# Kernel optimization log

Hardware: AMD Instinct MI355X
Metric: run time of the kernel (lower is better)

The kernel has to match this reference:

```python
import jax, jax.numpy as jnp
import numpy as np

D_MODEL = 1024
N_HEADS = 16
HEAD_DIM = D_MODEL // N_HEADS
B, S = 2, 2048


def setup_inputs() -> dict:
    key = jax.random.key(0)
    k1, k2, k3, k4, k5 = jax.random.split(key, 5)
    scale = 1.0 / np.sqrt(D_MODEL)
    return {
        "x": jax.random.normal(k1, (B, S, D_MODEL), dtype=jnp.float32),
        "mask": jnp.ones((B, S), dtype=jnp.int32),
        "W_qkv": jax.random.normal(k2, (D_MODEL, 3 * D_MODEL), dtype=jnp.float32) * scale,
        "b_qkv": jnp.zeros((3 * D_MODEL,), dtype=jnp.float32),
        "W_proj": jax.random.normal(k3, (D_MODEL, D_MODEL), dtype=jnp.float32) * scale,
        "b_proj": jnp.zeros((D_MODEL,), dtype=jnp.float32),
    }


def reference(x, mask, W_qkv, b_qkv, W_proj, b_proj):
    b, s, d = x.shape
    qkv = x @ W_qkv + b_qkv                                  # [B,S,3D]
    qkv = qkv.reshape(b, s, 3, N_HEADS, HEAD_DIM)
    qkv = jnp.transpose(qkv, (2, 0, 3, 1, 4))                # [3,B,H,S,Dh]
    q, k, v = qkv[0], qkv[1], qkv[2]
    scores = jnp.einsum("bhqd,bhkd->bhqk", q, k) / np.sqrt(HEAD_DIM)
    if mask is not None:
        m = mask[:, None, None, :]                           # [B,1,1,S]
        scores = jnp.where(m == 0, -jnp.inf, scores)
    attn = jax.nn.softmax(scores, axis=-1)
    out = jnp.einsum("bhqk,bhkd->bhqd", attn, v)             # [B,H,S,Dh]
    out = jnp.transpose(out, (0, 2, 1, 3)).reshape(b, s, d)  # [B,S,D]
    return out @ W_proj + b_proj
```

## Files before the change

### kernel.cpp

```cpp
#include <hip/hip_runtime.h>

typedef unsigned short u16;
typedef unsigned int u32;
typedef __bf16 bf16x8 __attribute__((ext_vector_type(8)));
typedef float f32x4 __attribute__((ext_vector_type(4)));
typedef float f32x16 __attribute__((ext_vector_type(16)));

#define D_MODEL 1024
#define SQ 2048
#define NH 16
#define HD 64
#define QSCALE 0.1803368801111204f

__device__ __forceinline__ u16 f2bf(float f) {
    u32 u = __builtin_bit_cast(u32, f);
    u = (u + 0x7fffu + ((u >> 16) & 1u)) >> 16;
    return (u16)u;
}

__device__ __forceinline__ f32x4 mfma16(bf16x8 a, bf16x8 b, f32x4 c) {
    return __builtin_amdgcn_mfma_f32_16x16x32_bf16(a, b, c, 0, 0, 0);
}
__device__ __forceinline__ f32x16 mfma32(bf16x8 a, bf16x8 b, f32x16 c) {
    return __builtin_amdgcn_mfma_f32_32x32x16_bf16(a, b, c, 0, 0, 0);
}

__device__ __forceinline__ bf16x8 ld16(const void* p) {
    return __builtin_bit_cast(bf16x8, *(const int4*)p);
}

__device__ __forceinline__ void gl_lds16(const u16* g, u16* l) {
    __builtin_amdgcn_global_load_lds((const __attribute__((address_space(1))) unsigned int*)g,
                                     (__attribute__((address_space(3))) unsigned int*)l, 16, 0, 0);
}

__device__ __forceinline__ u32 cvtpk(float a, float b) {
    u32 r;
    asm("v_cvt_pk_bf16_f32 %0, %1, %2" : "=v"(r) : "v"(a), "v"(b));
    return r;
}

__device__ __forceinline__ void swap32(u32& a, u32& b) {
    asm("v_permlane32_swap_b32 %0, %1" : "+v"(a), "+v"(b));
}

__device__ __forceinline__ void barrier_fence() {
    asm volatile("s_barrier" ::: "memory");
}


__global__ __launch_bounds__(256) void prep(const float* __restrict__ x, u16* __restrict__ x_bf,
                                            const float* __restrict__ Wqkv, u16* __restrict__ wq_t,
                                            const float* __restrict__ Wproj, u16* __restrict__ wp_t) {
    __shared__ float t[32][33];
    const int bid = blockIdx.x, tid = threadIdx.x;

    if (bid < 1024) {
#pragma unroll
        for (int j = 0; j < 4; ++j) {
            int i = bid * 1024 + j * 256 + tid;
            float4 v = ((const float4*)x)[i];
            ushort4 o;
            o.x = f2bf(v.x); o.y = f2bf(v.y); o.z = f2bf(v.z); o.w = f2bf(v.w);
            ((ushort4*)x_bf)[i] = o;
        }
        return;
    }

    const float* in;
    u16* out;
    int K = 1024, N, tile;
    if (bid < 4096) {
        in = Wqkv; out = wq_t; N = 3072; tile = bid - 1024;
    } else {
        in = Wproj; out = wp_t; N = 1024; tile = bid - 4096;
    }
    const int nbx = N / 32;
    const int n0 = (tile % nbx) * 32, k0 = (tile / nbx) * 32;
    const int tx = tid & 31, ty = tid >> 5;
#pragma unroll
    for (int i = 0; i < 4; ++i)
        t[ty + 8 * i][tx] = in[(size_t)(k0 + ty + 8 * i) * N + n0 + tx];
    __syncthreads();
#pragma unroll
    for (int i = 0; i < 4; ++i)
        out[(size_t)(n0 + ty + 8 * i) * K + k0 + tx] = f2bf(t[tx][ty + 8 * i]);
}

__global__ __launch_bounds__(256) void vtrans(const u16* __restrict__ Vw, u16* __restrict__ Vtw) {
    __shared__ u16 T[64][72];
    const int bh = blockIdx.y, s0 = blockIdx.x * 64, tid = threadIdx.x;
    const int r = tid >> 3, cb = tid & 7;
#pragma unroll
    for (int i = 0; i < 2; ++i) {
        int rr = r + 32 * i;
        int4 v = *(const int4*)(Vw + ((size_t)bh * SQ + s0 + rr) * HD + cb * 8);
        *(int4*)&T[rr][cb * 8] = v;
    }
    __syncthreads();
#pragma unroll
    for (int i = 0; i < 2; ++i) {
        int d = r + 32 * i, so = cb * 8;
        u16 tmp[8];
#pragma unroll
        for (int j = 0; j < 8; ++j) tmp[j] = T[so + j][d];
        *(int4*)(Vtw + ((size_t)bh * HD + d) * SQ + s0 + so) = *(int4*)tmp;
    }
}


template <int MODE>
__global__ __launch_bounds__(256) void gemm128(const u16* __restrict__ A,
                                               const u16* __restrict__ Bt,
                                               const float* __restrict__ bias,
                                               u16* __restrict__ Qw, u16* __restrict__ Kw,
                                               u16* __restrict__ Vw, float* __restrict__ Out) {
    __shared__ u16 As[128 * 32];
    __shared__ u16 Bs[128 * 32];

    const int tid = threadIdx.x;
    const int l = tid & 63, w = tid >> 6;
    const int l16 = l & 15, lq = l >> 4;
    const int wm = w >> 1, wn = w & 1;
    const int m0 = blockIdx.y * 128, n0 = blockIdx.x * 128;

    f32x4 acc[4][4];
#pragma unroll
    for (int i = 0; i < 4; ++i)
#pragma unroll
        for (int j = 0; j < 4; ++j) acc[i][j] = f32x4{0.f, 0.f, 0.f, 0.f};

    const int srow = 32 * w + (l >> 2);
    const u16* aSrc = A + (size_t)(m0 + srow) * 1024 + (l & 3) * 8;
    const u16* bSrc = Bt + (size_t)(n0 + srow) * 1024 + (l & 3) * 8;
    u16* AsW = As + w * 1024;
    u16* BsW = Bs + w * 1024;

    for (int kt = 0; kt < 32; ++kt) {
        __syncthreads();
        gl_lds16(aSrc + kt * 32, AsW);
        gl_lds16(aSrc + kt * 32 + (size_t)16 * 1024, AsW + 512);
        gl_lds16(bSrc + kt * 32, BsW);
        gl_lds16(bSrc + kt * 32 + (size_t)16 * 1024, BsW + 512);
        __syncthreads();

        bf16x8 af[4], bfr[4];
#pragma unroll
        for (int mi = 0; mi < 4; ++mi)
            af[mi] = ld16((char*)As + (wm * 64 + mi * 16 + l16) * 64 + lq * 16);
#pragma unroll
        for (int ni = 0; ni < 4; ++ni)
            bfr[ni] = ld16((char*)Bs + (wn * 64 + ni * 16 + l16) * 64 + lq * 16);
#pragma unroll
        for (int mi = 0; mi < 4; ++mi)
#pragma unroll
            for (int ni = 0; ni < 4; ++ni)
                acc[mi][ni] = mfma16(af[mi], bfr[ni], acc[mi][ni]);
    }

#pragma unroll
    for (int mi = 0; mi < 4; ++mi) {
#pragma unroll
        for (int ni = 0; ni < 4; ++ni) {
            const int n = n0 + wn * 64 + ni * 16 + l16;
            const float bv = bias[n];
#pragma unroll
            for (int r = 0; r < 4; ++r) {
                const int m = m0 + wm * 64 + mi * 16 + 4 * lq + r;
                float v = acc[mi][ni][r] + bv;
                if (MODE == 0) {
                    const int which = n >> 10;
                    const int h = (n >> 6) & 15;
                    const int d = n & 63;
                    const int b = m >> 11, s = m & 2047;
                    const size_t bh = (size_t)(b * NH + h);
                    if (which == 0)
                        Qw[(bh * SQ + s) * HD + d] = f2bf(v * QSCALE);
                    else if (which == 1)
                        Kw[(bh * SQ + s) * HD + d] = f2bf(v);
                    else
                        Vw[(bh * SQ + s) * HD + d] = f2bf(v);
                } else {
                    Out[(size_t)m * 1024 + n] = v;
                }
            }
        }
    }
}


__global__ __launch_bounds__(256) void gemm_proj(const u16* __restrict__ A,
                                                 const u16* __restrict__ Bt,
                                                 const float* __restrict__ bias,
                                                 float* __restrict__ Out) {
    __shared__ u16 As[128 * 32];
    __shared__ u16 Bs[64 * 32];

    const int tid = threadIdx.x;
    const int l = tid & 63, w = tid >> 6;
    const int l16 = l & 15, lq = l >> 4;
    const int wm = w >> 1, wn = w & 1;
    const int m0 = blockIdx.y * 128, n0 = blockIdx.x * 64;

    f32x4 acc[4][2];
#pragma unroll
    for (int i = 0; i < 4; ++i)
#pragma unroll
        for (int j = 0; j < 2; ++j) acc[i][j] = f32x4{0.f, 0.f, 0.f, 0.f};

    const int srowA = 32 * w + (l >> 2);
    const int srowB = 16 * w + (l >> 2);
    const u16* aSrc = A + (size_t)(m0 + srowA) * 1024 + (l & 3) * 8;
    const u16* bSrc = Bt + (size_t)(n0 + srowB) * 1024 + (l & 3) * 8;
    u16* AsW = As + w * 1024;
    u16* BsW = Bs + w * 512;

    for (int kt = 0; kt < 32; ++kt) {
        __syncthreads();
        gl_lds16(aSrc + kt * 32, AsW);
        gl_lds16(aSrc + kt * 32 + (size_t)16 * 1024, AsW + 512);
        gl_lds16(bSrc + kt * 32, BsW);
        __syncthreads();

        bf16x8 af[4], bfr[2];
#pragma unroll
        for (int mi = 0; mi < 4; ++mi)
            af[mi] = ld16((char*)As + (wm * 64 + mi * 16 + l16) * 64 + lq * 16);
#pragma unroll
        for (int ni = 0; ni < 2; ++ni)
            bfr[ni] = ld16((char*)Bs + (wn * 32 + ni * 16 + l16) * 64 + lq * 16);
#pragma unroll
        for (int mi = 0; mi < 4; ++mi)
#pragma unroll
            for (int ni = 0; ni < 2; ++ni)
                acc[mi][ni] = mfma16(af[mi], bfr[ni], acc[mi][ni]);
    }

#pragma unroll
    for (int mi = 0; mi < 4; ++mi) {
#pragma unroll
        for (int ni = 0; ni < 2; ++ni) {
            const int n = n0 + wn * 32 + ni * 16 + l16;
            const float bv = bias[n];
#pragma unroll
            for (int r = 0; r < 4; ++r) {
                const int m = m0 + wm * 64 + mi * 16 + 4 * lq + r;
                Out[(size_t)m * 1024 + n] = acc[mi][ni][r] + bv;
            }
        }
    }
}


__global__ __launch_bounds__(256, 4) void attn64(const u16* __restrict__ Qw, const u16* __restrict__ Kw,
                                                 const u16* __restrict__ Vtw, const int* __restrict__ mask,
                                                 u16* __restrict__ Ow) {
    __shared__ u16 Ks[2][64 * 64];
    __shared__ u16 Vs[2][64 * 64];
    __shared__ u16 smadd16[SQ];
    __shared__ int allFlag;

    const int tid = threadIdx.x;
    const int l = tid & 63, w = tid >> 6;
    const int q = l & 31, hl = l >> 5;
    const int qh = w & 1, kb = w >> 1;
    const int bh = blockIdx.y, b = bh >> 4, h = bh & 15;
    const int q0 = blockIdx.x * 64;

    if (tid == 0) allFlag = 1;
    __syncthreads();
    {
        const int4* m4 = (const int4*)(mask + (size_t)b * SQ) + tid * 2;
        int4 a0 = m4[0], a1 = m4[1];
        int ok = a0.x && a0.y && a0.z && a0.w && a1.x && a1.y && a1.z && a1.w;
        const u16 NEG = f2bf(-1e30f);
        u16* sp = &smadd16[tid * 8];
        sp[0] = a0.x ? (u16)0 : NEG; sp[1] = a0.y ? (u16)0 : NEG;
        sp[2] = a0.z ? (u16)0 : NEG; sp[3] = a0.w ? (u16)0 : NEG;
        sp[4] = a1.x ? (u16)0 : NEG; sp[5] = a1.y ? (u16)0 : NEG;
        sp[6] = a1.z ? (u16)0 : NEG; sp[7] = a1.w ? (u16)0 : NEG;
        if (!ok) allFlag = 0;
    }

    bf16x8 aq[4];
    {
        const u16* qb = Qw + ((size_t)bh * SQ + q0 + qh * 32 + q) * HD + hl * 8;
#pragma unroll
        for (int kc = 0; kc < 4; ++kc) aq[kc] = ld16(qb + kc * 16);
    }

    const int srow = l >> 3, scb = (l & 7) ^ srow;
    const u16* kbase = Kw + ((size_t)bh * SQ + 16 * w + srow) * HD + scb * 8;
    const u16* vbase = Vtw + ((size_t)bh * HD + 16 * w + srow) * SQ + scb * 8;

    __syncthreads();
    const bool anyMasked = (allFlag == 0);

    {
        u16* kd = (u16*)Ks[0] + w * 1024;
        u16* vd = (u16*)Vs[0] + w * 1024;
#pragma unroll
        for (int j = 0; j < 2; ++j) {
            gl_lds16(kbase + j * 8 * HD, kd + j * 512);
            gl_lds16(vbase + (size_t)j * 8 * SQ, vd + j * 512);
        }
    }

    f32x16 accO[2];
#pragma unroll
    for (int r = 0; r < 16; ++r) { accO[0][r] = 0.f; accO[1][r] = 0.f; }
    float ssum = 0.f;

    const int swzq = (q & 7) << 4;
    const int hb = hl * 16;
    const int krow = 32 * kb + q;

    int p = 0;
    for (int kt = 0; kt < SQ / 64; ++kt) {
        if (kt + 1 < SQ / 64) {
            u16* kd = (u16*)Ks[p ^ 1] + w * 1024;
            u16* vd = (u16*)Vs[p ^ 1] + w * 1024;
            const u16* ks = kbase + (size_t)(kt + 1) * 64 * HD;
            const u16* vs = vbase + (kt + 1) * 64;
#pragma unroll
            for (int j = 0; j < 2; ++j) {
                gl_lds16(ks + j * 8 * HD, kd + j * 512);
                gl_lds16(vs + (size_t)j * 8 * SQ, vd + j * 512);
            }
            asm volatile("s_waitcnt vmcnt(4)" ::: "memory");
        } else {
            asm volatile("s_waitcnt vmcnt(0)" ::: "memory");
        }
        barrier_fence();

        const char* Ksp = (const char*)Ks[p];
        const char* Vsp = (const char*)Vs[p];

        f32x16 s;
        if (anyMasked) {
#pragma unroll
            for (int r = 0; r < 16; ++r) {
                int key = kt * 64 + kb * 32 + (r & 3) + 8 * (r >> 2) + 4 * hl;
                u32 bits = (u32)smadd16[key] << 16;
                s[r] = __builtin_bit_cast(float, bits);
            }
        } else {
#pragma unroll
            for (int r = 0; r < 16; ++r) s[r] = 0.f;
        }

        __builtin_amdgcn_s_setprio(1);
#pragma unroll
        for (int kc = 0; kc < 4; ++kc) {
            bf16x8 kf = ld16(Ksp + krow * 128 + ((kc * 32 + hb) ^ swzq));
            s = mfma32(kf, aq[kc], s);
        }
        __builtin_amdgcn_s_setprio(0);

        u32 pw[4][2];
        float r0 = 0.f, r1 = 0.f, r2 = 0.f, r3 = 0.f;
#pragma unroll
        for (int q2 = 0; q2 < 4; ++q2) {
            float p0 = __builtin_amdgcn_exp2f(s[4 * q2 + 0]);
            float p1 = __builtin_amdgcn_exp2f(s[4 * q2 + 1]);
            float p2 = __builtin_amdgcn_exp2f(s[4 * q2 + 2]);
            float p3 = __builtin_amdgcn_exp2f(s[4 * q2 + 3]);
            r0 += p0; r1 += p1; r2 += p2; r3 += p3;
            pw[q2][0] = cvtpk(p0, p1);
            pw[q2][1] = cvtpk(p2, p3);
        }
        ssum += (r0 + r1) + (r2 + r3);

        bf16x8 pf[2];
#pragma unroll
        for (int c = 0; c < 2; ++c) {
            u32 x0 = pw[2 * c][0], y0 = pw[2 * c + 1][0];
            u32 x1 = pw[2 * c][1], y1 = pw[2 * c + 1][1];
            swap32(x0, y0);
            swap32(x1, y1);
            int4 f;
            f.x = x0; f.y = x1; f.z = y0; f.w = y1;
            pf[c] = __builtin_bit_cast(bf16x8, f);
        }

        __builtin_amdgcn_s_setprio(1);
#pragma unroll
        for (int db = 0; db < 2; ++db) {
            const int vrow = 32 * db + q;
#pragma unroll
            for (int c = 0; c < 2; ++c) {
                bf16x8 vf = ld16(Vsp + vrow * 128 + ((kb * 64 + c * 32 + hb) ^ swzq));
                accO[db] = mfma32(vf, pf[c], accO[db]);
            }
        }
        __builtin_amdgcn_s_setprio(0);

        barrier_fence();
        p ^= 1;
    }

    ssum += __shfl_xor(ssum, 32);

    if (w >= 2) {
        float* ssx = (float*)Vs;
        ssx[qh * 64 + l] = ssum;
        int4* ex = (int4*)Ks + qh * 512 + l;
#pragma unroll
        for (int ch = 0; ch < 8; ++ch) {
            f32x4 qd;
#pragma unroll
            for (int t = 0; t < 4; ++t) qd[t] = accO[ch >> 2][(ch & 3) * 4 + t];
            ex[ch * 64] = __builtin_bit_cast(int4, qd);
        }
    }
    __syncthreads();
    if (w < 2) {
        const float stot = ssum + ((const float*)Vs)[w * 64 + l];
        const float inv = stot > 0.f ? 1.f / stot : 0.f;
        const int4* ex = (const int4*)Ks + w * 512 + l;
#pragma unroll
        for (int ch = 0; ch < 8; ++ch) {
            f32x4 a = __builtin_bit_cast(f32x4, ex[ch * 64]);
#pragma unroll
            for (int t = 0; t < 4; ++t) accO[ch >> 2][(ch & 3) * 4 + t] += a[t];
        }

        u16* ot = (u16*)Vs + 512 + w * 2048;
#pragma unroll
        for (int db = 0; db < 2; ++db)
#pragma unroll
            for (int m = 0; m < 4; ++m) {
                u32 w0 = cvtpk(accO[db][4 * m + 0] * inv, accO[db][4 * m + 1] * inv);
                u32 w1 = cvtpk(accO[db][4 * m + 2] * inv, accO[db][4 * m + 3] * inv);
                const int dbase = 32 * db + 8 * m + 4 * hl;
                uint2 pr; pr.x = w0; pr.y = w1;
                *(uint2*)((char*)ot + q * 128 + ((dbase * 2) ^ ((q & 7) << 4))) = pr;
            }
#pragma unroll
        for (int i = 0; i < 4; ++i) {
            const int qr = 8 * i + (l >> 3);
            int4 vv = *(const int4*)((char*)ot + qr * 128 + (((l & 7) * 16) ^ ((qr & 7) << 4)));
            *(int4*)(Ow + ((size_t)b * SQ + q0 + 32 * w + qr) * D_MODEL + h * HD + (l & 7) * 8) = vv;
        }
    }
}


extern "C" void kernel_launch(void* const* d_in, const int* in_sizes, int n_in,
                              void* d_out, int out_size, void* d_ws, size_t ws_size,
                              hipStream_t stream) {
    (void)in_sizes; (void)n_in; (void)out_size; (void)ws_size;
    const float* x = (const float*)d_in[0];
    const int* mask = (const int*)d_in[1];
    const float* Wqkv = (const float*)d_in[2];
    const float* bqkv = (const float*)d_in[3];
    const float* Wproj = (const float*)d_in[4];
    const float* bproj = (const float*)d_in[5];
    float* out = (float*)d_out;

    char* ws = (char*)d_ws;
    const size_t MB = 1024 * 1024;
    u16* x_bf = (u16*)(ws);
    u16* wq_t = (u16*)(ws + 8 * MB);
    u16* wp_t = (u16*)(ws + 14 * MB);
    u16* Qw   = (u16*)(ws + 16 * MB);
    u16* Kw   = (u16*)(ws + 24 * MB);
    u16* Vtw  = (u16*)(ws + 32 * MB);
    u16* Ow   = (u16*)(ws + 40 * MB);
    u16* Vw   = (u16*)(ws + 40 * MB);

    prep<<<5120, 256, 0, stream>>>(x, x_bf, Wqkv, wq_t, Wproj, wp_t);
    gemm128<0><<<dim3(24, 32), 256, 0, stream>>>(x_bf, wq_t, bqkv, Qw, Kw, Vw, nullptr);
    vtrans<<<dim3(32, 32), 256, 0, stream>>>(Vw, Vtw);
    attn64<<<dim3(32, 32), 256, 0, stream>>>(Qw, Kw, Vtw, mask, Ow);
    gemm_proj<<<dim3(16, 32), 256, 0, stream>>>(Ow, wp_t, bproj, out);
}
```

Baseline: 195.7 us.

## Load K/V fragments straight from global into registers, dropping LDS staging and barriers

The attention loop no longer stages K and V^T tiles in double-buffered LDS through cooperative global_load_lds and per-iteration barriers. Each wave now loads its own MFMA operand fragments directly from global memory into registers. The LDS is reduced to a small buffer used only for the final cross-wave combine of the two key halves. This removes the two barriers per iteration and the LDS read traffic. In exchange, each K/V fragment is fetched by both query-half waves, the accesses are less coalesced, and load latency is exposed because there is no explicit prefetch of the next tile.

```diff
diff --git a/kernel.cpp b/kernel.cpp
--- a/kernel.cpp
+++ b/kernel.cpp
@@ -42,10 +42,6 @@
 
 __device__ __forceinline__ void swap32(u32& a, u32& b) {
     asm("v_permlane32_swap_b32 %0, %1" : "+v"(a), "+v"(b));
-}
-
-__device__ __forceinline__ void barrier_fence() {
-    asm volatile("s_barrier" ::: "memory");
 }
 
 
@@ -255,8 +251,8 @@
 __global__ __launch_bounds__(256, 4) void attn64(const u16* __restrict__ Qw, const u16* __restrict__ Kw,
                                                  const u16* __restrict__ Vtw, const int* __restrict__ mask,
                                                  u16* __restrict__ Ow) {
-    __shared__ u16 Ks[2][64 * 64];
-    __shared__ u16 Vs[2][64 * 64];
+    __shared__ float comb[2][64 * 32];
+    __shared__ float ssx[128];
     __shared__ u16 smadd16[SQ];
     __shared__ int allFlag;
 
@@ -289,52 +285,25 @@
         for (int kc = 0; kc < 4; ++kc) aq[kc] = ld16(qb + kc * 16);
     }
 
-    const int srow = l >> 3, scb = (l & 7) ^ srow;
-    const u16* kbase = Kw + ((size_t)bh * SQ + 16 * w + srow) * HD + scb * 8;
-    const u16* vbase = Vtw + ((size_t)bh * HD + 16 * w + srow) * SQ + scb * 8;
+    const u16* kP = Kw + ((size_t)bh * SQ + 32 * kb + q) * HD + 8 * hl;
+    const u16* vP0 = Vtw + ((size_t)bh * HD + q) * SQ + 32 * kb + 8 * hl;
+    const u16* vP1 = vP0 + (size_t)32 * SQ;
 
     __syncthreads();
     const bool anyMasked = (allFlag == 0);
 
-    {
-        u16* kd = (u16*)Ks[0] + w * 1024;
-        u16* vd = (u16*)Vs[0] + w * 1024;
-#pragma unroll
-        for (int j = 0; j < 2; ++j) {
-            gl_lds16(kbase + j * 8 * HD, kd + j * 512);
-            gl_lds16(vbase + (size_t)j * 8 * SQ, vd + j * 512);
-        }
-    }
-
     f32x16 accO[2];
 #pragma unroll
     for (int r = 0; r < 16; ++r) { accO[0][r] = 0.f; accO[1][r] = 0.f; }
     float ssum = 0.f;
 
-    const int swzq = (q & 7) << 4;
-    const int hb = hl * 16;
-    const int krow = 32 * kb + q;
-
-    int p = 0;
     for (int kt = 0; kt < SQ / 64; ++kt) {
-        if (kt + 1 < SQ / 64) {
-            u16* kd = (u16*)Ks[p ^ 1] + w * 1024;
-            u16* vd = (u16*)Vs[p ^ 1] + w * 1024;
-            const u16* ks = kbase + (size_t)(kt + 1) * 64 * HD;
-            const u16* vs = vbase + (kt + 1) * 64;
-#pragma unroll
-            for (int j = 0; j < 2; ++j) {
-                gl_lds16(ks + j * 8 * HD, kd + j * 512);
-                gl_lds16(vs + (size_t)j * 8 * SQ, vd + j * 512);
-            }
-            asm volatile("s_waitcnt vmcnt(4)" ::: "memory");
-        } else {
-            asm volatile("s_waitcnt vmcnt(0)" ::: "memory");
-        }
-        barrier_fence();
-
-        const char* Ksp = (const char*)Ks[p];
-        const char* Vsp = (const char*)Vs[p];
+        bf16x8 kf0 = ld16(kP), kf1 = ld16(kP + 16), kf2 = ld16(kP + 32), kf3 = ld16(kP + 48);
+        bf16x8 vf00 = ld16(vP0), vf01 = ld16(vP0 + 16);
+        bf16x8 vf10 = ld16(vP1), vf11 = ld16(vP1 + 16);
+        kP += 64 * HD;
+        vP0 += 64;
+        vP1 += 64;
 
         f32x16 s;
         if (anyMasked) {
@@ -350,11 +319,10 @@
         }
 
         __builtin_amdgcn_s_setprio(1);
-#pragma unroll
-        for (int kc = 0; kc < 4; ++kc) {
-            bf16x8 kf = ld16(Ksp + krow * 128 + ((kc * 32 + hb) ^ swzq));
-            s = mfma32(kf, aq[kc], s);
-        }
+        s = mfma32(kf0, aq[0], s);
+        s = mfma32(kf1, aq[1], s);
+        s = mfma32(kf2, aq[2], s);
+        s = mfma32(kf3, aq[3], s);
         __builtin_amdgcn_s_setprio(0);
 
         u32 pw[4][2];
@@ -384,27 +352,18 @@
         }
 
         __builtin_amdgcn_s_setprio(1);
-#pragma unroll
-        for (int db = 0; db < 2; ++db) {
-            const int vrow = 32 * db + q;
-#pragma unroll
-            for (int c = 0; c < 2; ++c) {
-                bf16x8 vf = ld16(Vsp + vrow * 128 + ((kb * 64 + c * 32 + hb) ^ swzq));
-                accO[db] = mfma32(vf, pf[c], accO[db]);
-            }
-        }
+        accO[0] = mfma32(vf00, pf[0], accO[0]);
+        accO[0] = mfma32(vf01, pf[1], accO[0]);
+        accO[1] = mfma32(vf10, pf[0], accO[1]);
+        accO[1] = mfma32(vf11, pf[1], accO[1]);
         __builtin_amdgcn_s_setprio(0);
-
-        barrier_fence();
-        p ^= 1;
     }
 
     ssum += __shfl_xor(ssum, 32);
 
-    if (w >= 2) {
-        float* ssx = (float*)Vs;
+    if (kb == 0) {
         ssx[qh * 64 + l] = ssum;
-        int4* ex = (int4*)Ks + qh * 512 + l;
+        int4* ex = (int4*)comb + qh * 512 + l;
 #pragma unroll
         for (int ch = 0; ch < 8; ++ch) {
             f32x4 qd;
@@ -414,18 +373,19 @@
         }
     }
     __syncthreads();
-    if (w < 2) {
-        const float stot = ssum + ((const float*)Vs)[w * 64 + l];
+    if (kb == 1) {
+        const float stot = ssum + ssx[qh * 64 + l];
         const float inv = stot > 0.f ? 1.f / stot : 0.f;
-        const int4* ex = (const int4*)Ks + w * 512 + l;
+        const int4* ex = (const int4*)comb + qh * 512 + l;
 #pragma unroll
         for (int ch = 0; ch < 8; ++ch) {
             f32x4 a = __builtin_bit_cast(f32x4, ex[ch * 64]);
 #pragma unroll
             for (int t = 0; t < 4; ++t) accO[ch >> 2][(ch & 3) * 4 + t] += a[t];
         }
-
-        u16* ot = (u16*)Vs + 512 + w * 2048;
+        asm volatile("s_waitcnt lgkmcnt(0)" ::: "memory");
+
+        u16* ot = (u16*)comb + qh * 4096;
 #pragma unroll
         for (int db = 0; db < 2; ++db)
 #pragma unroll
@@ -440,7 +400,7 @@
         for (int i = 0; i < 4; ++i) {
             const int qr = 8 * i + (l >> 3);
             int4 vv = *(const int4*)((char*)ot + qr * 128 + (((l & 7) * 16) ^ ((qr & 7) << 4)));
-            *(int4*)(Ow + ((size_t)b * SQ + q0 + 32 * w + qr) * D_MODEL + h * HD + (l & 7) * 8) = vv;
+            *(int4*)(Ow + ((size_t)b * SQ + q0 + qh * 32 + qr) * D_MODEL + h * HD + (l & 7) * 8) = vv;
         }
     }
 }
```

Result: slower. 264.5 us (+35.2%).
